# Optimization experiments

Measured on AMD Instinct MI355X. Metric: run time of the kernel, lower is better.

The kernel has to match this reference:

```python
import jax, jax.numpy as jnp
import numpy as np

B, T, C, H = 4, 2048, 768, 12
HS = C // H

def setup_inputs() -> dict:
    key = jax.random.key(0)
    ks = jax.random.split(key, 5)
    s = 0.02
    return {
        "x": jax.random.normal(ks[0], (B, T, C), jnp.float32),
        "W_attn": jax.random.normal(ks[1], (C, 3 * C), jnp.float32) * s,
        "b_attn": jnp.zeros((3 * C,), jnp.float32),
        "W_proj": jax.random.normal(ks[2], (C, C), jnp.float32) * s,
        "b_proj": jnp.zeros((C,), jnp.float32),
    }

def reference(x, W_attn, b_attn, W_proj, b_proj):
    Bz, Tz, Cz = x.shape
    qkv = x @ W_attn + b_attn                       # [B,T,3C]
    q, k, v = jnp.split(qkv, 3, axis=-1)
    # [B,T,C] -> [B,H,T,HS]
    def heads(t):
        return t.reshape(Bz, Tz, H, HS).transpose(0, 2, 1, 3)
    q, k, v = heads(q), heads(k), heads(v)
    scale = 1.0 / jnp.sqrt(jnp.asarray(HS, x.dtype))
    att = jnp.einsum("bhqd,bhkd->bhqk", q, k) * scale  # [B,H,T,T]
    causal = jnp.tril(jnp.ones((Tz, Tz), bool))
    att = jnp.where(causal[None, None], att, -jnp.inf)
    att = jax.nn.softmax(att, axis=-1)
    y = jnp.einsum("bhqk,bhkd->bhqd", att, v)       # [B,H,T,HS]
    y = y.transpose(0, 2, 1, 3).reshape(Bz, Tz, Cz)
    return y @ W_proj + b_proj
```

## Files before the change

### kernel.cpp

```cpp
#include <hip/hip_runtime.h>
#include <hip/hip_bf16.h>


typedef short s16x8 __attribute__((ext_vector_type(8)));
typedef float f32x4 __attribute__((ext_vector_type(4)));
typedef unsigned short u16x4 __attribute__((ext_vector_type(4)));
typedef unsigned short u16x8 __attribute__((ext_vector_type(8)));

#define MFMA16 __builtin_amdgcn_mfma_f32_16x16x32_bf16

__device__ __forceinline__ unsigned short f2bf(float f) {
    union { float f; unsigned u; } v; v.f = f;
    unsigned r = v.u + 0x7FFFu + ((v.u >> 16) & 1u);
    return (unsigned short)(r >> 16);
}

__device__ __forceinline__ void gload16(const unsigned short* g, unsigned short* l) {
    __builtin_amdgcn_global_load_lds(
        (__attribute__((address_space(1))) void*)(const void*)g,
        (__attribute__((address_space(3))) void*)l, 16, 0, 0);
}

__global__ __launch_bounds__(256) void cvt_f32_bf16(
    const float* __restrict__ src, unsigned short* __restrict__ dst, int n4)
{
    int i = blockIdx.x * 256 + threadIdx.x;
    if (i >= n4) return;
    float4 v = reinterpret_cast<const float4*>(src)[i];
    u16x4 o = { f2bf(v.x), f2bf(v.y), f2bf(v.z), f2bf(v.w) };
    reinterpret_cast<u16x4*>(dst)[i] = o;
}

__global__ __launch_bounds__(256) void cvt_transpose(
    const float* __restrict__ src, unsigned short* __restrict__ dst, int R, int C)
{
    __shared__ unsigned short tile[32][33];
    const int c0 = blockIdx.x * 32, r0 = blockIdx.y * 32;
    const int tx = threadIdx.x & 31, ty = threadIdx.x >> 5;
#pragma unroll
    for (int j = 0; j < 32; j += 8)
        tile[ty + j][tx] = f2bf(src[(size_t)(r0 + ty + j) * C + c0 + tx]);
    __syncthreads();
#pragma unroll
    for (int j = 0; j < 32; j += 8)
        dst[(size_t)(c0 + ty + j) * R + r0 + tx] = tile[tx][ty + j];
}

template<bool SCALEQ, bool OUT_BF16>
__global__ __launch_bounds__(256, 2) void gemm_bt(
    const unsigned short* __restrict__ A, const unsigned short* __restrict__ Bt,
    const float* __restrict__ bias, void* __restrict__ Cout,
    int M, int N, int K)
{
    __shared__ unsigned short lds_a[128 * 32];
    __shared__ unsigned short lds_b[128 * 32];

    const int tid = threadIdx.x, lane = tid & 63, w = tid >> 6;
    const int wr = w >> 1, wc = w & 1;
    const int m0 = blockIdx.y * 128, n0 = blockIdx.x * 128;
    const int lr = lane & 15, lg = lane >> 4;

    f32x4 acc[4][4];
#pragma unroll
    for (int mi = 0; mi < 4; ++mi)
#pragma unroll
        for (int ni = 0; ni < 4; ++ni)
            acc[mi][ni] = f32x4{0.f, 0.f, 0.f, 0.f};

    const int sr = tid >> 2, sc = (tid & 3) * 8;
    const unsigned short* Ap = A  + (size_t)(m0 + sr) * K + sc;
    const unsigned short* Aq = A  + (size_t)(m0 + 64 + sr) * K + sc;
    const unsigned short* Bp = Bt + (size_t)(n0 + sr) * K + sc;
    const unsigned short* Bq = Bt + (size_t)(n0 + 64 + sr) * K + sc;
    unsigned short* la0 = lds_a + (w << 9);
    unsigned short* la1 = lds_a + 2048 + (w << 9);
    unsigned short* lb0 = lds_b + (w << 9);
    unsigned short* lb1 = lds_b + 2048 + (w << 9);

    for (int k0 = 0; k0 < K; k0 += 32) {
        gload16(Ap + k0, la0);
        gload16(Aq + k0, la1);
        gload16(Bp + k0, lb0);
        gload16(Bq + k0, lb1);
        __syncthreads();

        s16x8 af[4], bfr[4];
#pragma unroll
        for (int mi = 0; mi < 4; ++mi)
            af[mi] = *reinterpret_cast<const s16x8*>(&lds_a[(wr * 64 + mi * 16 + lr) * 32 + lg * 8]);
#pragma unroll
        for (int ni = 0; ni < 4; ++ni)
            bfr[ni] = *reinterpret_cast<const s16x8*>(&lds_b[(wc * 64 + ni * 16 + lr) * 32 + lg * 8]);
#pragma unroll
        for (int mi = 0; mi < 4; ++mi)
#pragma unroll
            for (int ni = 0; ni < 4; ++ni)
                acc[mi][ni] = MFMA16(af[mi], bfr[ni], acc[mi][ni], 0, 0, 0);
        __syncthreads();
    }

#pragma unroll
    for (int ni = 0; ni < 4; ++ni) {
        int col = n0 + wc * 64 + ni * 16 + lr;
        float bs = bias[col];
        float scq = (SCALEQ && col < 768) ? 0.18033688011112042f : 1.0f;
#pragma unroll
        for (int mi = 0; mi < 4; ++mi)
#pragma unroll
            for (int r = 0; r < 4; ++r) {
                int row = m0 + wr * 64 + mi * 16 + lg * 4 + r;
                float v = (acc[mi][ni][r] + bs) * scq;
                if (OUT_BF16)
                    ((unsigned short*)Cout)[(size_t)row * N + col] = f2bf(v);
                else
                    ((float*)Cout)[(size_t)row * N + col] = v;
            }
    }
}

__global__ __launch_bounds__(256, 2) void attn_fwd(
    const unsigned short* __restrict__ qkv, unsigned short* __restrict__ att)
{
    __shared__ unsigned short lds_k[64 * 72];
    __shared__ unsigned short lds_v[64 * 72];
    __shared__ unsigned short lds_p[4][32 * 72];

    const int tid = threadIdx.x, lane = tid & 63, w = tid >> 6;
    const int lr = lane & 15, lg = lane >> 4;
    const int bh = blockIdx.x;
    const int qt = 15 - blockIdx.y;
    const int b = bh / 12, h = bh % 12;
    const size_t bT = (size_t)b * 2048;
    const int q0 = qt * 128;
    const int wq = q0 + w * 32;

    s16x8 qf[2][2];
#pragma unroll
    for (int mi = 0; mi < 2; ++mi) {
        const size_t qoff = (bT + wq + mi * 16 + lr) * 2304 + h * 64 + lg * 8;
        qf[mi][0] = *reinterpret_cast<const s16x8*>(qkv + qoff);
        qf[mi][1] = *reinterpret_cast<const s16x8*>(qkv + qoff + 32);
    }

    f32x4 o[2][4];
    f32x4 lsum[2];
#pragma unroll
    for (int mi = 0; mi < 2; ++mi) {
        lsum[mi] = f32x4{0.f, 0.f, 0.f, 0.f};
#pragma unroll
        for (int dt = 0; dt < 4; ++dt) o[mi][dt] = f32x4{0.f, 0.f, 0.f, 0.f};
    }

    const int ksr = tid >> 2, ksc = (tid & 3) * 16;
    const int vd = tid & 63;
    const int nkt = 2 * (qt + 1);

    for (int kt = 0; kt < nkt; ++kt) {
        const int kv0 = kt * 64;
        {
            const unsigned short* kp = qkv + (bT + kv0 + ksr) * 2304 + 768 + h * 64 + ksc;
            u16x8 k0 = *reinterpret_cast<const u16x8*>(kp);
            u16x8 k1 = *reinterpret_cast<const u16x8*>(kp + 8);
            *reinterpret_cast<u16x8*>(&lds_k[ksr * 72 + ksc]) = k0;
            *reinterpret_cast<u16x8*>(&lds_k[ksr * 72 + ksc + 8]) = k1;
        }
        {
            const unsigned short* vp0 = qkv + (bT + kv0) * 2304 + 1536 + h * 64 + vd;
#pragma unroll
            for (int it = 0; it < 2; ++it) {
                int k8 = it * 32 + w * 8;
                const unsigned short* vp = vp0 + (size_t)k8 * 2304;
                u16x8 pk = { vp[0], vp[2304], vp[4608], vp[6912],
                             vp[9216], vp[11520], vp[13824], vp[16128] };
                *reinterpret_cast<u16x8*>(&lds_v[vd * 72 + k8]) = pk;
            }
        }
        __syncthreads();

        f32x4 sf[2][4];
#pragma unroll
        for (int mi = 0; mi < 2; ++mi)
#pragma unroll
            for (int n = 0; n < 4; ++n) sf[mi][n] = f32x4{0.f, 0.f, 0.f, 0.f};
#pragma unroll
        for (int kk = 0; kk < 2; ++kk)
#pragma unroll
            for (int n = 0; n < 4; ++n) {
                s16x8 kf = *reinterpret_cast<const s16x8*>(&lds_k[(n * 16 + lr) * 72 + kk * 32 + lg * 8]);
                sf[0][n] = MFMA16(qf[0][kk], kf, sf[0][n], 0, 0, 0);
                sf[1][n] = MFMA16(qf[1][kk], kf, sf[1][n], 0, 0, 0);
            }

        if (kv0 + 63 > wq) {
#pragma unroll
            for (int mi = 0; mi < 2; ++mi)
#pragma unroll
                for (int n = 0; n < 4; ++n)
#pragma unroll
                    for (int r = 0; r < 4; ++r) {
                        int key = kv0 + n * 16 + lr;
                        int row = wq + mi * 16 + lg * 4 + r;
                        if (key > row) sf[mi][n][r] = -1.0e30f;
                    }
        }

#pragma unroll
        for (int mi = 0; mi < 2; ++mi)
#pragma unroll
            for (int n = 0; n < 4; ++n) {
                f32x4 p;
#pragma unroll
                for (int r = 0; r < 4; ++r) p[r] = __builtin_amdgcn_exp2f(sf[mi][n][r]);
                lsum[mi] += p;
#pragma unroll
                for (int r = 0; r < 4; ++r)
                    lds_p[w][(mi * 16 + lg * 4 + r) * 72 + n * 16 + lr] = f2bf(p[r]);
            }

#pragma unroll
        for (int kk = 0; kk < 2; ++kk) {
            s16x8 pf0 = *reinterpret_cast<const s16x8*>(&lds_p[w][(lr) * 72 + kk * 32 + lg * 8]);
            s16x8 pf1 = *reinterpret_cast<const s16x8*>(&lds_p[w][(16 + lr) * 72 + kk * 32 + lg * 8]);
#pragma unroll
            for (int dt = 0; dt < 4; ++dt) {
                s16x8 vf = *reinterpret_cast<const s16x8*>(&lds_v[(dt * 16 + lr) * 72 + kk * 32 + lg * 8]);
                o[0][dt] = MFMA16(pf0, vf, o[0][dt], 0, 0, 0);
                o[1][dt] = MFMA16(pf1, vf, o[1][dt], 0, 0, 0);
            }
        }
        __syncthreads();
    }

#pragma unroll
    for (int mi = 0; mi < 2; ++mi)
#pragma unroll
        for (int mask = 1; mask < 16; mask <<= 1)
#pragma unroll
            for (int r = 0; r < 4; ++r)
                lsum[mi][r] += __shfl_xor(lsum[mi][r], mask);

#pragma unroll
    for (int mi = 0; mi < 2; ++mi)
#pragma unroll
        for (int dt = 0; dt < 4; ++dt)
#pragma unroll
            for (int r = 0; r < 4; ++r) {
                int row = wq + mi * 16 + lg * 4 + r;
                att[(bT + row) * 768 + h * 64 + dt * 16 + lr] = f2bf(o[mi][dt][r] / lsum[mi][r]);
            }
}

extern "C" void kernel_launch(void* const* d_in, const int* in_sizes, int n_in,
                              void* d_out, int out_size, void* d_ws, size_t ws_size,
                              hipStream_t stream) {
    const float* x      = (const float*)d_in[0];
    const float* W_attn = (const float*)d_in[1];
    const float* b_attn = (const float*)d_in[2];
    const float* W_proj = (const float*)d_in[3];
    const float* b_proj = (const float*)d_in[4];

    unsigned short* ws    = (unsigned short*)d_ws;
    unsigned short* x_bf  = ws;
    unsigned short* wa_t  = x_bf + 6291456;
    unsigned short* wp_t  = wa_t + 1769472;
    unsigned short* qkv   = wp_t + 589824;
    unsigned short* att   = qkv + 18874368;

    cvt_f32_bf16<<<6144, 256, 0, stream>>>(x, x_bf, 6291456 / 4);
    cvt_transpose<<<dim3(72, 24), 256, 0, stream>>>(W_attn, wa_t, 768, 2304);
    cvt_transpose<<<dim3(24, 24), 256, 0, stream>>>(W_proj, wp_t, 768, 768);

    gemm_bt<true , true ><<<dim3(18, 64), 256, 0, stream>>>(x_bf, wa_t, b_attn, qkv, 8192, 2304, 768);
    attn_fwd<<<dim3(48, 16), 256, 0, stream>>>(qkv, att);
    gemm_bt<false, false><<<dim3(6, 64), 256, 0, stream>>>(att, wp_t, b_proj, d_out, 8192, 768, 768);
}
```

Measured before the change: 238.4 us.

## Prefetch K/V into registers, swizzle LDS layouts, skip fully masked tiles

The attention loop now loads the next K/V tile into registers while the current tile is being computed. V is read with coalesced 16-byte loads and transposed through scalar LDS stores with a row-skewed layout, replacing strided 2-byte global gathers. The P and V LDS accesses are XOR-swizzled or offset to reduce bank conflicts. Warps whose query rows are entirely masked for a tile now skip the compute, and launch bounds are raised to 4 blocks per CU. The risks are extra register pressure from the prefetch buffers and a possible occupancy change.

```diff
diff --git a/kernel.cpp b/kernel.cpp
--- a/kernel.cpp
+++ b/kernel.cpp
@@ -118,11 +118,11 @@
     }
 }
 
-__global__ __launch_bounds__(256, 2) void attn_fwd(
+__global__ __launch_bounds__(256, 4) void attn_fwd(
     const unsigned short* __restrict__ qkv, unsigned short* __restrict__ att)
 {
     __shared__ unsigned short lds_k[64 * 72];
-    __shared__ unsigned short lds_v[64 * 72];
+    __shared__ unsigned short lds_v[64 * 72 + 64];
     __shared__ unsigned short lds_p[4][32 * 72];
 
     const int tid = threadIdx.x, lane = tid & 63, w = tid >> 6;
@@ -151,81 +151,99 @@
         for (int dt = 0; dt < 4; ++dt) o[mi][dt] = f32x4{0.f, 0.f, 0.f, 0.f};
     }
 
-    const int ksr = tid >> 2, ksc = (tid & 3) * 16;
-    const int vd = tid & 63;
+    const int sr = tid >> 2, sc = (tid & 3) * 16;
+    const unsigned short* kbase = qkv + (bT + sr) * 2304 + 768 + h * 64 + sc;
+    const unsigned short* vbase = qkv + (bT + sr) * 2304 + 1536 + h * 64 + sc;
+    unsigned short* kdst = &lds_k[sr * 72 + sc];
+    unsigned short* vdst = &lds_v[sc * 72 + ((sc >> 3) & 7) * 8 + sr];
+    const int lrx = lr ^ ((lg & 1) << 3);
+    const int nb16 = ((lg >> 1) & 1) << 4;
+    const int rsel = ((lr >> 2) & 3) << 3;
+
     const int nkt = 2 * (qt + 1);
+
+    u16x8 kr0, kr1, vr0, vr1;
+    kr0 = *reinterpret_cast<const u16x8*>(kbase);
+    kr1 = *reinterpret_cast<const u16x8*>(kbase + 8);
+    vr0 = *reinterpret_cast<const u16x8*>(vbase);
+    vr1 = *reinterpret_cast<const u16x8*>(vbase + 8);
 
     for (int kt = 0; kt < nkt; ++kt) {
         const int kv0 = kt * 64;
+        *reinterpret_cast<u16x8*>(kdst)     = kr0;
+        *reinterpret_cast<u16x8*>(kdst + 8) = kr1;
+#pragma unroll
+        for (int jj = 0; jj < 8; ++jj)
+            vdst[jj * 72 + (jj >> 3) * 8] = vr0[jj];
+#pragma unroll
+        for (int jj = 8; jj < 16; ++jj)
+            vdst[jj * 72 + (jj >> 3) * 8] = vr1[jj - 8];
+        __syncthreads();
+
         {
-            const unsigned short* kp = qkv + (bT + kv0 + ksr) * 2304 + 768 + h * 64 + ksc;
-            u16x8 k0 = *reinterpret_cast<const u16x8*>(kp);
-            u16x8 k1 = *reinterpret_cast<const u16x8*>(kp + 8);
-            *reinterpret_cast<u16x8*>(&lds_k[ksr * 72 + ksc]) = k0;
-            *reinterpret_cast<u16x8*>(&lds_k[ksr * 72 + ksc + 8]) = k1;
+            const int ktn = (kt + 1 < nkt) ? kt + 1 : kt;
+            const size_t off = (size_t)(ktn * 64) * 2304;
+            kr0 = *reinterpret_cast<const u16x8*>(kbase + off);
+            kr1 = *reinterpret_cast<const u16x8*>(kbase + off + 8);
+            vr0 = *reinterpret_cast<const u16x8*>(vbase + off);
+            vr1 = *reinterpret_cast<const u16x8*>(vbase + off + 8);
         }
-        {
-            const unsigned short* vp0 = qkv + (bT + kv0) * 2304 + 1536 + h * 64 + vd;
-#pragma unroll
-            for (int it = 0; it < 2; ++it) {
-                int k8 = it * 32 + w * 8;
-                const unsigned short* vp = vp0 + (size_t)k8 * 2304;
-                u16x8 pk = { vp[0], vp[2304], vp[4608], vp[6912],
-                             vp[9216], vp[11520], vp[13824], vp[16128] };
-                *reinterpret_cast<u16x8*>(&lds_v[vd * 72 + k8]) = pk;
-            }
-        }
-        __syncthreads();
-
-        f32x4 sf[2][4];
-#pragma unroll
-        for (int mi = 0; mi < 2; ++mi)
-#pragma unroll
-            for (int n = 0; n < 4; ++n) sf[mi][n] = f32x4{0.f, 0.f, 0.f, 0.f};
-#pragma unroll
-        for (int kk = 0; kk < 2; ++kk)
-#pragma unroll
-            for (int n = 0; n < 4; ++n) {
-                s16x8 kf = *reinterpret_cast<const s16x8*>(&lds_k[(n * 16 + lr) * 72 + kk * 32 + lg * 8]);
-                sf[0][n] = MFMA16(qf[0][kk], kf, sf[0][n], 0, 0, 0);
-                sf[1][n] = MFMA16(qf[1][kk], kf, sf[1][n], 0, 0, 0);
-            }
-
-        if (kv0 + 63 > wq) {
+
+        if (kv0 <= wq + 31) {
+            f32x4 sf[2][4];
 #pragma unroll
             for (int mi = 0; mi < 2; ++mi)
 #pragma unroll
-                for (int n = 0; n < 4; ++n)
-#pragma unroll
-                    for (int r = 0; r < 4; ++r) {
-                        int key = kv0 + n * 16 + lr;
-                        int row = wq + mi * 16 + lg * 4 + r;
-                        if (key > row) sf[mi][n][r] = -1.0e30f;
-                    }
-        }
-
-#pragma unroll
-        for (int mi = 0; mi < 2; ++mi)
-#pragma unroll
-            for (int n = 0; n < 4; ++n) {
-                f32x4 p;
-#pragma unroll
-                for (int r = 0; r < 4; ++r) p[r] = __builtin_amdgcn_exp2f(sf[mi][n][r]);
-                lsum[mi] += p;
-#pragma unroll
-                for (int r = 0; r < 4; ++r)
-                    lds_p[w][(mi * 16 + lg * 4 + r) * 72 + n * 16 + lr] = f2bf(p[r]);
-            }
-
-#pragma unroll
-        for (int kk = 0; kk < 2; ++kk) {
-            s16x8 pf0 = *reinterpret_cast<const s16x8*>(&lds_p[w][(lr) * 72 + kk * 32 + lg * 8]);
-            s16x8 pf1 = *reinterpret_cast<const s16x8*>(&lds_p[w][(16 + lr) * 72 + kk * 32 + lg * 8]);
-#pragma unroll
-            for (int dt = 0; dt < 4; ++dt) {
-                s16x8 vf = *reinterpret_cast<const s16x8*>(&lds_v[(dt * 16 + lr) * 72 + kk * 32 + lg * 8]);
-                o[0][dt] = MFMA16(pf0, vf, o[0][dt], 0, 0, 0);
-                o[1][dt] = MFMA16(pf1, vf, o[1][dt], 0, 0, 0);
+                for (int n = 0; n < 4; ++n) sf[mi][n] = f32x4{0.f, 0.f, 0.f, 0.f};
+#pragma unroll
+            for (int kk = 0; kk < 2; ++kk)
+#pragma unroll
+                for (int n = 0; n < 4; ++n) {
+                    s16x8 kf = *reinterpret_cast<const s16x8*>(&lds_k[(n * 16 + lr) * 72 + kk * 32 + lg * 8]);
+                    sf[0][n] = MFMA16(qf[0][kk], kf, sf[0][n], 0, 0, 0);
+                    sf[1][n] = MFMA16(qf[1][kk], kf, sf[1][n], 0, 0, 0);
+                }
+
+            if (kv0 + 63 > wq) {
+#pragma unroll
+                for (int mi = 0; mi < 2; ++mi)
+#pragma unroll
+                    for (int n = 0; n < 4; ++n)
+#pragma unroll
+                        for (int r = 0; r < 4; ++r) {
+                            int key = kv0 + n * 16 + lr;
+                            int row = wq + mi * 16 + lg * 4 + r;
+                            if (key > row) sf[mi][n][r] = -1.0e30f;
+                        }
+            }
+
+#pragma unroll
+            for (int mi = 0; mi < 2; ++mi)
+#pragma unroll
+                for (int n = 0; n < 4; ++n) {
+                    f32x4 p;
+#pragma unroll
+                    for (int r = 0; r < 4; ++r) p[r] = __builtin_amdgcn_exp2f(sf[mi][n][r]);
+                    lsum[mi] += p;
+                    const int kx = ((n << 4) ^ nb16) + lrx;
+#pragma unroll
+                    for (int r = 0; r < 4; ++r)
+                        lds_p[w][(mi * 16 + lg * 4 + r) * 72 + kx] = f2bf(p[r]);
+                }
+
+#pragma unroll
+            for (int kk = 0; kk < 2; ++kk) {
+                const int pko = (kk * 32 + lg * 8) ^ rsel;
+                s16x8 pf0 = *reinterpret_cast<const s16x8*>(&lds_p[w][lr * 72 + pko]);
+                s16x8 pf1 = *reinterpret_cast<const s16x8*>(&lds_p[w][(16 + lr) * 72 + pko]);
+#pragma unroll
+                for (int dt = 0; dt < 4; ++dt) {
+                    const int vrow = dt * 16 + lr;
+                    s16x8 vf = *reinterpret_cast<const s16x8*>(
+                        &lds_v[vrow * 72 + ((vrow >> 3) & 7) * 8 + kk * 32 + lg * 8]);
+                    o[0][dt] = MFMA16(pf0, vf, o[0][dt], 0, 0, 0);
+                    o[1][dt] = MFMA16(pf1, vf, o[1][dt], 0, 0, 0);
+                }
             }
         }
         __syncthreads();
```

Measured after the change: 223.2 us. -6.4%, faster.
